# Performance work log

Measured on AMD Instinct MI355X. Metric: run time of the kernel, lower is better.

The kernel has to match this reference:

```python
import jax, jax.numpy as jnp
import numpy as np

B, D_IN, T = 16, 1024, 4096
CB_SIZE, CB_DIM = 1024, 8
EPS = 1e-12  # F.normalize eps


def _wn_weight(v, g):
    # weight_norm over dim=0: per-output-row normalization. v: [out, in], g: [out]
    return g[:, None] * v / jnp.linalg.norm(v, axis=1, keepdims=True)


def setup_inputs() -> dict:
    key = jax.random.key(0)
    ks = jax.random.split(key, 8)
    z = jax.random.normal(ks[0], (B, D_IN, T), dtype=jnp.float32)
    in_v = jax.random.normal(ks[1], (CB_DIM, D_IN), dtype=jnp.float32) * 0.02
    in_g = jnp.linalg.norm(in_v, axis=1)  # weight_norm init: g = ||v||
    in_b = jnp.zeros((CB_DIM,), dtype=jnp.float32)
    out_v = jax.random.normal(ks[2], (D_IN, CB_DIM), dtype=jnp.float32) * 0.02
    out_g = jnp.linalg.norm(out_v, axis=1)
    out_b = jnp.zeros((D_IN,), dtype=jnp.float32)
    codebook = jax.random.normal(ks[3], (CB_SIZE, CB_DIM), dtype=jnp.float32)
    return {"z": z, "in_v": in_v, "in_g": in_g, "in_b": in_b,
            "out_v": out_v, "out_g": out_g, "out_b": out_b, "codebook": codebook}


def reference(z, in_v, in_g, in_b, out_v, out_g, out_b, codebook):
    # in_proj: 1x1 weight-normed conv, z: [B, D_IN, T] -> z_e: [B, CB_DIM, T]
    w_in = _wn_weight(in_v, in_g)
    z_e = jnp.einsum('od,bdt->bot', w_in, z) + in_b[None, :, None]

    # decode_latents: (b t) d tokens, L2-normalize, cosine distance, argmin
    enc = z_e.transpose(0, 2, 1).reshape(-1, CB_DIM)              # [(B*T), CB_DIM]
    enc_n = enc / jnp.maximum(jnp.linalg.norm(enc, axis=1, keepdims=True), EPS)
    cb_n = codebook / jnp.maximum(jnp.linalg.norm(codebook, axis=1, keepdims=True), EPS)
    dist = (jnp.sum(enc_n ** 2, axis=1, keepdims=True)
            - 2.0 * enc_n @ cb_n.T
            + jnp.sum(cb_n ** 2, axis=1)[None, :])                # [(B*T), CB_SIZE]
    indices = jnp.argmax(-dist, axis=1).reshape(B, T)             # argmin of dist
    z_q = codebook[indices].transpose(0, 2, 1)                    # [B, CB_DIM, T]

    commitment_loss = jnp.mean((z_e - jax.lax.stop_gradient(z_q)) ** 2, axis=(1, 2))
    codebook_loss = jnp.mean((z_q - jax.lax.stop_gradient(z_e)) ** 2, axis=(1, 2))

    # straight-through estimator
    z_q_st = z_e + jax.lax.stop_gradient(z_q - z_e)

    # out_proj: 1x1 weight-normed conv back to input_dim
    w_out = _wn_weight(out_v, out_g)
    z_out = jnp.einsum('od,bdt->bot', w_out, z_q_st) + out_b[None, :, None]
    return (z_out, commitment_loss, codebook_loss, indices, z_e)
```

## Files before the change

kernel.cpp:

```cpp
#include <hip/hip_runtime.h>
#include <math.h>


namespace {
constexpr int kB  = 16;
constexpr int kD  = 1024;
constexpr int kT  = 4096;
constexpr int kCB = 1024;
constexpr int kC  = 8;
constexpr float kEps = 1e-12f;

constexpr size_t N_ZOUT    = (size_t)kB * kD * kT;
constexpr size_t OFF_COMMIT = N_ZOUT;
constexpr size_t OFF_CBL    = OFF_COMMIT + kB;
constexpr size_t OFF_IDX    = OFF_CBL + kB;
constexpr size_t OFF_ZE     = OFF_IDX + (size_t)kB * kT;
}

__global__ void vq_prep(const float* __restrict__ in_v, const float* __restrict__ in_g,
                        const float* __restrict__ out_v, const float* __restrict__ out_g,
                        const float* __restrict__ cb,
                        float* __restrict__ w_in_t, float* __restrict__ w_out_t,
                        float* __restrict__ cb_n_t)
{
    __shared__ float red[4];
    const int blk = blockIdx.x;
    const int tid = threadIdx.x;
    if (blk < 8) {
        const int o = blk;
        float ss = 0.f;
        for (int d = tid; d < kD; d += 256) {
            float v = in_v[o * kD + d];
            ss = fmaf(v, v, ss);
        }
        #pragma unroll
        for (int off = 32; off; off >>= 1) ss += __shfl_xor(ss, off);
        if ((tid & 63) == 0) red[tid >> 6] = ss;
        __syncthreads();
        const float scale = in_g[o] / sqrtf(red[0] + red[1] + red[2] + red[3]);
        for (int d = tid; d < kD; d += 256)
            w_in_t[d * kC + o] = scale * in_v[o * kD + d];
    } else if (blk < 12) {
        const int r = (blk - 8) * 256 + tid;
        float4 a = reinterpret_cast<const float4*>(cb)[2 * r];
        float4 b = reinterpret_cast<const float4*>(cb)[2 * r + 1];
        float n = sqrtf(a.x*a.x + a.y*a.y + a.z*a.z + a.w*a.w +
                        b.x*b.x + b.y*b.y + b.z*b.z + b.w*b.w);
        float s = 1.f / fmaxf(n, kEps);
        a.x *= s; a.y *= s; a.z *= s; a.w *= s;
        b.x *= s; b.y *= s; b.z *= s; b.w *= s;
        reinterpret_cast<float4*>(cb_n_t)[2 * r]     = a;
        reinterpret_cast<float4*>(cb_n_t)[2 * r + 1] = b;
    } else {
        const int r = (blk - 12) * 256 + tid;
        float4 a = reinterpret_cast<const float4*>(out_v)[2 * r];
        float4 b = reinterpret_cast<const float4*>(out_v)[2 * r + 1];
        float n = sqrtf(a.x*a.x + a.y*a.y + a.z*a.z + a.w*a.w +
                        b.x*b.x + b.y*b.y + b.z*b.z + b.w*b.w);
        float s = out_g[r] / n;
        a.x *= s; a.y *= s; a.z *= s; a.w *= s;
        b.x *= s; b.y *= s; b.z *= s; b.w *= s;
        reinterpret_cast<float4*>(w_out_t)[2 * r]     = a;
        reinterpret_cast<float4*>(w_out_t)[2 * r + 1] = b;
    }
}

__global__ __launch_bounds__(256, 4)
void vq_main(const float* __restrict__ z,
             const float* __restrict__ in_b, const float* __restrict__ out_b,
             const float* __restrict__ cb,
             const float* __restrict__ w_in_t, const float* __restrict__ w_out_t,
             const float* __restrict__ cb_n_t,
             float* __restrict__ out)
{
    __shared__ float s_red[4][kC][64];
    __shared__ float s_ze[kC][64];
    __shared__ float s_zq[kC][64];
    __shared__ float s_sim[16][64];
    __shared__ int   s_idx[16][64];

    const int tid = threadIdx.x;
    const int tg = tid & 15;
    const int sl = tid >> 4;
    const int wv = tid >> 6;
    const int g0 = blockIdx.x * 64;
    const int b  = g0 >> 12;
    const int t0 = g0 & (kT - 1);

    const float* zp = z + ((size_t)b * kD + (size_t)sl * 64) * kT + t0 + 4 * tg;
    const float4* wq = reinterpret_cast<const float4*>(w_in_t) + (size_t)sl * 128;
    float acc[kC][4];
    #pragma unroll
    for (int c = 0; c < kC; c++)
        #pragma unroll
        for (int j = 0; j < 4; j++) acc[c][j] = 0.f;

    #pragma unroll 4
    for (int i = 0; i < 64; i++) {
        const float4 zv = *reinterpret_cast<const float4*>(zp + (size_t)i * kT);
        const float4 w0 = wq[2 * i];
        const float4 w1 = wq[2 * i + 1];
        const float zl[4] = {zv.x, zv.y, zv.z, zv.w};
        const float wl[kC] = {w0.x, w0.y, w0.z, w0.w, w1.x, w1.y, w1.z, w1.w};
        #pragma unroll
        for (int c = 0; c < kC; c++)
            #pragma unroll
            for (int j = 0; j < 4; j++)
                acc[c][j] = fmaf(zl[j], wl[c], acc[c][j]);
    }
    #pragma unroll
    for (int c = 0; c < kC; c++)
        #pragma unroll
        for (int j = 0; j < 4; j++) {
            float v = acc[c][j];
            v += __shfl_xor(v, 16);
            v += __shfl_xor(v, 32);
            acc[c][j] = v;
        }
    if ((tid & 48) == 0) {
        #pragma unroll
        for (int c = 0; c < kC; c++)
            #pragma unroll
            for (int j = 0; j < 4; j++) s_red[wv][c][4 * tg + j] = acc[c][j];
    }
    __syncthreads();

    {
        const int c  = tid >> 5;
        const int t2 = (tid & 31) * 2;
        #pragma unroll
        for (int k = 0; k < 2; k++) {
            const int t = t2 + k;
            s_ze[c][t] = s_red[0][c][t] + s_red[1][c][t] + s_red[2][c][t]
                       + s_red[3][c][t] + in_b[c];
        }
    }
    __syncthreads();

    float zef[4][kC];
    #pragma unroll
    for (int j = 0; j < 4; j++)
        #pragma unroll
        for (int c = 0; c < kC; c++) zef[j][c] = s_ze[c][4 * tg + j];

    float best[4] = {-INFINITY, -INFINITY, -INFINITY, -INFINITY};
    int   bk[4]   = {sl * 64, sl * 64, sl * 64, sl * 64};
    const float4* cq = reinterpret_cast<const float4*>(cb_n_t) + (size_t)sl * 128;
    #pragma unroll 2
    for (int i = 0; i < 64; i++) {
        const float4 c0 = cq[2 * i];
        const float4 c1 = cq[2 * i + 1];
        const float cl[kC] = {c0.x, c0.y, c0.z, c0.w, c1.x, c1.y, c1.z, c1.w};
        #pragma unroll
        for (int j = 0; j < 4; j++) {
            float sim = zef[j][0] * cl[0];
            #pragma unroll
            for (int c = 1; c < kC; c++) sim = fmaf(zef[j][c], cl[c], sim);
            if (sim > best[j]) { best[j] = sim; bk[j] = sl * 64 + i; }
        }
    }
    #pragma unroll
    for (int j = 0; j < 4; j++) {
        s_sim[sl][4 * tg + j] = best[j];
        s_idx[sl][4 * tg + j] = bk[j];
    }
    __syncthreads();

    if (tid < 64) {
        const int t = tid;
        float bs = s_sim[0][t];
        int   bi = s_idx[0][t];
        #pragma unroll
        for (int g = 1; g < 16; g++) {
            const float v = s_sim[g][t];
            if (v > bs) { bs = v; bi = s_idx[g][t]; }
        }
        out[OFF_IDX + (size_t)b * kT + t0 + t] = (float)bi;

        const float4 q0 = reinterpret_cast<const float4*>(cb)[2 * bi];
        const float4 q1 = reinterpret_cast<const float4*>(cb)[2 * bi + 1];
        const float zq[kC] = {q0.x, q0.y, q0.z, q0.w, q1.x, q1.y, q1.z, q1.w};

        float lsum = 0.f;
        #pragma unroll
        for (int c = 0; c < kC; c++) {
            s_zq[c][t] = zq[c];
            const float ze = s_ze[c][t];
            const float d = ze - zq[c];
            lsum = fmaf(d, d, lsum);
            out[OFF_ZE + (size_t)b * (kC * kT) + (size_t)c * kT + t0 + t] = ze;
        }
        #pragma unroll
        for (int off = 32; off; off >>= 1) lsum += __shfl_xor(lsum, off);
        if (tid == 0) {
            const float lv = lsum * (1.f / (kC * kT));
            atomicAdd(&out[OFF_COMMIT + b], lv);
            atomicAdd(&out[OFF_CBL + b], lv);
        }
    }
    __syncthreads();

    float zqr[4][kC];
    #pragma unroll
    for (int j = 0; j < 4; j++)
        #pragma unroll
        for (int c = 0; c < kC; c++) zqr[j][c] = s_zq[c][4 * tg + j];

    const float4* wo = reinterpret_cast<const float4*>(w_out_t) + (size_t)sl * 128;
    const float*  bo = out_b + sl * 64;
    float* op = out + ((size_t)b * kD + (size_t)sl * 64) * kT + t0 + 4 * tg;
    #pragma unroll 4
    for (int i = 0; i < 64; i++) {
        const float4 w0 = wo[2 * i];
        const float4 w1 = wo[2 * i + 1];
        const float wl[kC] = {w0.x, w0.y, w0.z, w0.w, w1.x, w1.y, w1.z, w1.w};
        const float bias = bo[i];
        float rr[4];
        #pragma unroll
        for (int j = 0; j < 4; j++) {
            float v = bias;
            #pragma unroll
            for (int c = 0; c < kC; c++) v = fmaf(zqr[j][c], wl[c], v);
            rr[j] = v;
        }
        const float4 r = make_float4(rr[0], rr[1], rr[2], rr[3]);
        *reinterpret_cast<float4*>(op + (size_t)i * kT) = r;
    }
}

extern "C" void kernel_launch(void* const* d_in, const int* in_sizes, int n_in,
                              void* d_out, int out_size, void* d_ws, size_t ws_size,
                              hipStream_t stream) {
    const float* z     = (const float*)d_in[0];
    const float* in_v  = (const float*)d_in[1];
    const float* in_g  = (const float*)d_in[2];
    const float* in_b  = (const float*)d_in[3];
    const float* out_v = (const float*)d_in[4];
    const float* out_g = (const float*)d_in[5];
    const float* out_b = (const float*)d_in[6];
    const float* cb    = (const float*)d_in[7];
    float* out = (float*)d_out;

    float* w_in_t  = (float*)d_ws;
    float* w_out_t = w_in_t + (size_t)kD * kC;
    float* cb_n_t  = w_out_t + (size_t)kD * kC;

    vq_prep<<<16, 256, 0, stream>>>(in_v, in_g, out_v, out_g, cb,
                                    w_in_t, w_out_t, cb_n_t);
    (void)hipMemsetAsync(out + OFF_COMMIT, 0, 2 * kB * sizeof(float), stream);
    vq_main<<<(kB * kT) / 64, 256, 0, stream>>>(z, in_b, out_b, cb,
                                                w_in_t, w_out_t, cb_n_t, out);
}
```

Measured before the change: 522.9 us.

## Split out-projection into a separate kernel with row-contiguous writes

The fused kernel is split in two. The encode kernel now writes z_q to a workspace buffer. A new vq_out kernel then computes the output projection one full output row at a time, so each block writes a contiguous 16 KB row instead of the strided 64-float segments the fused version produced. The goal is better write coalescing and DRAM locality on the roughly 268 MB output store, at the cost of an extra kernel launch and an extra workspace round trip for z_q (about 2 MB, which should stay mostly cache-resident).

```diff
diff --git a/kernel.cpp b/kernel.cpp
--- a/kernel.cpp
+++ b/kernel.cpp
@@ -65,17 +65,17 @@
     }
 }
 
-__global__ __launch_bounds__(256, 4)
-void vq_main(const float* __restrict__ z,
-             const float* __restrict__ in_b, const float* __restrict__ out_b,
-             const float* __restrict__ cb,
-             const float* __restrict__ w_in_t, const float* __restrict__ w_out_t,
-             const float* __restrict__ cb_n_t,
-             float* __restrict__ out)
+__global__ __launch_bounds__(256)
+void vq_encode(const float* __restrict__ z,
+               const float* __restrict__ in_b,
+               const float* __restrict__ cb,
+               const float* __restrict__ w_in_t,
+               const float* __restrict__ cb_n_t,
+               float* __restrict__ zq_ws,
+               float* __restrict__ out)
 {
     __shared__ float s_red[4][kC][64];
     __shared__ float s_ze[kC][64];
-    __shared__ float s_zq[kC][64];
     __shared__ float s_sim[16][64];
     __shared__ int   s_idx[16][64];
 
@@ -184,11 +184,11 @@
         float lsum = 0.f;
         #pragma unroll
         for (int c = 0; c < kC; c++) {
-            s_zq[c][t] = zq[c];
             const float ze = s_ze[c][t];
             const float d = ze - zq[c];
             lsum = fmaf(d, d, lsum);
             out[OFF_ZE + (size_t)b * (kC * kT) + (size_t)c * kT + t0 + t] = ze;
+            zq_ws[((size_t)b * kC + c) * kT + t0 + t] = zq[c];
         }
         #pragma unroll
         for (int off = 32; off; off >>= 1) lsum += __shfl_xor(lsum, off);
@@ -198,33 +198,43 @@
             atomicAdd(&out[OFF_CBL + b], lv);
         }
     }
-    __syncthreads();
-
-    float zqr[4][kC];
-    #pragma unroll
-    for (int j = 0; j < 4; j++)
-        #pragma unroll
-        for (int c = 0; c < kC; c++) zqr[j][c] = s_zq[c][4 * tg + j];
-
-    const float4* wo = reinterpret_cast<const float4*>(w_out_t) + (size_t)sl * 128;
-    const float*  bo = out_b + sl * 64;
-    float* op = out + ((size_t)b * kD + (size_t)sl * 64) * kT + t0 + 4 * tg;
-    #pragma unroll 4
-    for (int i = 0; i < 64; i++) {
-        const float4 w0 = wo[2 * i];
-        const float4 w1 = wo[2 * i + 1];
+}
+
+__global__ __launch_bounds__(256)
+void vq_out(const float* __restrict__ zq_ws,
+            const float* __restrict__ w_out_t, const float* __restrict__ out_b,
+            float* __restrict__ out)
+{
+    const int tid = threadIdx.x;
+    for (int row = blockIdx.x; row < kB * kD; row += gridDim.x) {
+        const int b = row >> 10;
+        const int o = row & (kD - 1);
+        const float4 w0 = reinterpret_cast<const float4*>(w_out_t)[2 * o];
+        const float4 w1 = reinterpret_cast<const float4*>(w_out_t)[2 * o + 1];
         const float wl[kC] = {w0.x, w0.y, w0.z, w0.w, w1.x, w1.y, w1.z, w1.w};
-        const float bias = bo[i];
-        float rr[4];
-        #pragma unroll
-        for (int j = 0; j < 4; j++) {
-            float v = bias;
-            #pragma unroll
-            for (int c = 0; c < kC; c++) v = fmaf(zqr[j][c], wl[c], v);
-            rr[j] = v;
-        }
-        const float4 r = make_float4(rr[0], rr[1], rr[2], rr[3]);
-        *reinterpret_cast<float4*>(op + (size_t)i * kT) = r;
+        const float bias = out_b[o];
+        const float4* zqp = reinterpret_cast<const float4*>(zq_ws)
+                          + (size_t)b * kC * (kT / 4);
+        float4* op = reinterpret_cast<float4*>(out) + (size_t)row * (kT / 4);
+        #pragma unroll
+        for (int k = 0; k < 4; k++) {
+            const int t4 = k * 256 + tid;
+            float q[kC][4];
+            #pragma unroll
+            for (int c = 0; c < kC; c++) {
+                const float4 qv = zqp[c * (kT / 4) + t4];
+                q[c][0] = qv.x; q[c][1] = qv.y; q[c][2] = qv.z; q[c][3] = qv.w;
+            }
+            float rr[4];
+            #pragma unroll
+            for (int j = 0; j < 4; j++) {
+                float v = bias;
+                #pragma unroll
+                for (int c = 0; c < kC; c++) v = fmaf(q[c][j], wl[c], v);
+                rr[j] = v;
+            }
+            op[t4] = make_float4(rr[0], rr[1], rr[2], rr[3]);
+        }
     }
 }
 
@@ -244,10 +254,12 @@
     float* w_in_t  = (float*)d_ws;
     float* w_out_t = w_in_t + (size_t)kD * kC;
     float* cb_n_t  = w_out_t + (size_t)kD * kC;
+    float* zq_ws   = cb_n_t + (size_t)kCB * kC;
 
     vq_prep<<<16, 256, 0, stream>>>(in_v, in_g, out_v, out_g, cb,
                                     w_in_t, w_out_t, cb_n_t);
     (void)hipMemsetAsync(out + OFF_COMMIT, 0, 2 * kB * sizeof(float), stream);
-    vq_main<<<(kB * kT) / 64, 256, 0, stream>>>(z, in_b, out_b, cb,
-                                                w_in_t, w_out_t, cb_n_t, out);
-}
+    vq_encode<<<(kB * kT) / 64, 256, 0, stream>>>(z, in_b, cb, w_in_t, cb_n_t,
+                                                  zq_ws, out);
+    vq_out<<<2048, 256, 0, stream>>>(zq_ws, w_out_t, out_b, out);
+}
```

After: 526.5 us. No clear change (+0.7%).
